# Optimization experiments

Measured on AMD Instinct MI355X. Metric: run time of the kernel, lower is better.

Reference implementation:

```python
import jax, jax.numpy as jnp
import numpy as np

B, N, IN_F, OUT_F = 32, 1024, 256, 256
ALPHA = 0.2  # LeakyReLU negative slope
NEG_INF = -9e15  # matches torch's -9000000000000000.0 masking constant


def setup_inputs() -> dict:
    key = jax.random.key(0)
    k1, k2, k3, k4 = jax.random.split(key, 4)
    h = jax.random.normal(k1, (B, N, IN_F), dtype=jnp.float32)
    adj = jax.random.randint(k2, (B, N, N), 0, 2, dtype=jnp.int32)
    W = jax.random.normal(k3, (OUT_F, IN_F), dtype=jnp.float32) * 0.05
    a = jax.random.normal(k4, (1, 2 * OUT_F), dtype=jnp.float32) * 0.05
    return {"h": h, "adj": adj, "W": W, "a": a}


def reference(h, adj, W, a):
    # Wh: (B, N, out)
    Wh = jnp.einsum("bni,oi->bno", h, W)
    # Decompose a([Wh_i || Wh_j]) = Wh_i . a1 + Wh_j . a2 (identical math,
    # avoids the O(B*N^2*2*out) concat intermediate of the torch code).
    a1 = a[0, :OUT_F]   # (out,)
    a2 = a[0, OUT_F:]   # (out,)
    si = Wh @ a1        # (B, N) score contribution of source node i
    sj = Wh @ a2        # (B, N) score contribution of neighbor node j
    e = jax.nn.leaky_relu(si[:, :, None] + sj[:, None, :], negative_slope=ALPHA)
    attention = jnp.where(adj > 0, e, NEG_INF)
    attention = jax.nn.softmax(attention, axis=-1)
    # dropout omitted (eval mode)
    h_prime = jnp.einsum("bij,bjo->bio", attention, Wh)
    return jax.nn.elu(h_prime)
```

## Files before the change

### kernel.cpp

```cpp
#include <hip/hip_runtime.h>
#include <hip/hip_bf16.h>


#define ALPHA 0.2f
#define LOG2E 1.44269504f

typedef __bf16 bf16x8 __attribute__((ext_vector_type(8)));
typedef __bf16 bf16x4 __attribute__((ext_vector_type(4)));
typedef float  f32x4  __attribute__((ext_vector_type(4)));
typedef unsigned long long u64;

__global__ __launch_bounds__(256) void k1_gemm1(const float* __restrict__ h,
                                                const float* __restrict__ W,
                                                const float* __restrict__ a_g,
                                                __bf16* __restrict__ whT,
                                                float* __restrict__ si,
                                                float* __restrict__ sj) {
    __shared__ __bf16 hA[64 * 72];
    __shared__ __bf16 hB[256 * 72];
    __shared__ float  red[512];
    const int t    = threadIdx.x;
    const int r0   = blockIdx.x * 64;
    const int b    = r0 >> 10;
    const int n0   = r0 & 1023;
    const int w    = t >> 6;
    const int l    = t & 63;
    const int ln   = l & 15;
    const int quad = l >> 4;

    f32x4 acc[4][4] = {};
    float4 ha_r[4], wb_r[16];

    #pragma unroll
    for (int it = 0; it < 4; ++it)
        ha_r[it] = *(const float4*)&h[(size_t)(r0 + it * 16 + (t >> 4)) * 256 + (t & 15) * 4];
    #pragma unroll
    for (int it = 0; it < 16; ++it)
        wb_r[it] = *(const float4*)&W[(size_t)(it * 16 + (t >> 4)) * 256 + (t & 15) * 4];

    for (int kc = 0; kc < 4; ++kc) {
        #pragma unroll
        for (int it = 0; it < 4; ++it) {
            const float4 v = ha_r[it];
            bf16x4 pv = {(__bf16)v.x, (__bf16)v.y, (__bf16)v.z, (__bf16)v.w};
            *(bf16x4*)&hA[(it * 16 + (t >> 4)) * 72 + (t & 15) * 4] = pv;
        }
        #pragma unroll
        for (int it = 0; it < 16; ++it) {
            const float4 v = wb_r[it];
            bf16x4 pv = {(__bf16)v.x, (__bf16)v.y, (__bf16)v.z, (__bf16)v.w};
            *(bf16x4*)&hB[(it * 16 + (t >> 4)) * 72 + (t & 15) * 4] = pv;
        }
        __syncthreads();
        if (kc < 3) {
            const int k0 = (kc + 1) * 64;
            #pragma unroll
            for (int it = 0; it < 4; ++it)
                ha_r[it] = *(const float4*)&h[(size_t)(r0 + it * 16 + (t >> 4)) * 256 + k0 + (t & 15) * 4];
            #pragma unroll
            for (int it = 0; it < 16; ++it)
                wb_r[it] = *(const float4*)&W[(size_t)(it * 16 + (t >> 4)) * 256 + k0 + (t & 15) * 4];
        }
        #pragma unroll
        for (int kk = 0; kk < 2; ++kk) {
            bf16x8 af[4], bfr[4];
            #pragma unroll
            for (int ri = 0; ri < 4; ++ri)
                af[ri] = *(const bf16x8*)&hA[(ri * 16 + ln) * 72 + kk * 32 + quad * 8];
            #pragma unroll
            for (int oi = 0; oi < 4; ++oi)
                bfr[oi] = *(const bf16x8*)&hB[(w * 64 + oi * 16 + ln) * 72 + kk * 32 + quad * 8];
            #pragma unroll
            for (int ri = 0; ri < 4; ++ri)
                #pragma unroll
                for (int oi = 0; oi < 4; ++oi)
                    acc[ri][oi] = __builtin_amdgcn_mfma_f32_16x16x32_bf16(
                        af[ri], bfr[oi], acc[ri][oi], 0, 0, 0);
        }
        __syncthreads();
    }

    #pragma unroll
    for (int ri = 0; ri < 4; ++ri) {
        const int n = ri * 16 + quad * 4;
        #pragma unroll
        for (int oi = 0; oi < 4; ++oi) {
            const int o = w * 64 + oi * 16 + ln;
            bf16x4 pv = {(__bf16)acc[ri][oi][0], (__bf16)acc[ri][oi][1],
                         (__bf16)acc[ri][oi][2], (__bf16)acc[ri][oi][3]};
            *(bf16x4*)&hB[o * 72 + n] = pv;
        }
    }
    __syncthreads();

    #pragma unroll
    for (int it = 0; it < 8; ++it) {
        const int o   = w * 64 + it * 8 + (l >> 3);
        const int seg = l & 7;
        const bf16x8 v = *(const bf16x8*)&hB[o * 72 + seg * 8];
        *(bf16x8*)&whT[((size_t)b * 256 + o) * 1024 + n0 + seg * 8] = v;
    }

    {
        float s1 = 0.f, s2 = 0.f;
        #pragma unroll 8
        for (int oi = 0; oi < 64; ++oi) {
            const int o = w * 64 + oi;
            const float v = (float)hB[o * 72 + l];
            s1 += v * a_g[o];
            s2 += v * a_g[256 + o];
        }
        red[w * 64 + l]       = s1;
        red[256 + w * 64 + l] = s2;
    }
    __syncthreads();
    if (t < 64) {
        si[b * 1024 + n0 + t] =
            (red[t] + red[64 + t] + red[128 + t] + red[192 + t]) * LOG2E;
    } else if (t < 128) {
        const int n = t - 64;
        sj[b * 1024 + n0 + n] =
            (red[256 + n] + red[320 + n] + red[384 + n] + red[448 + n]) * LOG2E;
    }
}

#define K3_BODY(JC, A0C, A1C, SJC, A0N, A1N, SJN)                              \
  {                                                                            \
    const int j0 = (JC) * 64;                                                  \
       \
    _Pragma("unroll")                                                          \
    for (int it = 0; it < 4; ++it)                                             \
      *(bf16x8*)&lds_w[(it * 64 + (t >> 3)) * 72 + (t & 7) * 8] = vreg[it];    \
              \
    if ((JC) < 15) {                                                           \
      _Pragma("unroll")                                                        \
      for (int it = 0; it < 4; ++it)                                           \
        vreg[it] = *(const bf16x8*)&whTb[                                      \
            (size_t)(it * 64 + (t >> 3)) * 1024 + j0 + 64 + (t & 7) * 8];      \
      A0N = *(const int4*)&adjb[(size_t)rowg * 1024 + j0 + 64 + j4 * 4];       \
      A1N = *(const int4*)&adjb[(size_t)(rowg + 32) * 1024 + j0 + 64 + j4 * 4];\
      SJN = *(const float4*)&sj_g[bs + j0 + 64 + j4 * 4];                      \
    }                                                                          \
         \
    {                                                                          \
      float e0 = si0 + SJC.x; e0 = fmaxf(e0, ALPHA * e0);                      \
      float e1 = si0 + SJC.y; e1 = fmaxf(e1, ALPHA * e1);                      \
      float e2 = si0 + SJC.z; e2 = fmaxf(e2, ALPHA * e2);                      \
      float e3 = si0 + SJC.w; e3 = fmaxf(e3, ALPHA * e3);                      \
      const float w0 = A0C.x > 0 ? exp2f(e0) : 0.f;                            \
      const float w1 = A0C.y > 0 ? exp2f(e1) : 0.f;                            \
      const float w2 = A0C.z > 0 ? exp2f(e2) : 0.f;                            \
      const float w3 = A0C.w > 0 ? exp2f(e3) : 0.f;                            \
      bf16x4 pv = {(__bf16)w0, (__bf16)w1, (__bf16)w2, (__bf16)w3};            \
      dsum0 += (float)pv[0] + (float)pv[1] + (float)pv[2] + (float)pv[3];      \
      *(bf16x4*)&lds_s[rowg * 72 + j4 * 4] = pv;                               \
    }                                                                          \
    {                                                                          \
      float e0 = si1 + SJC.x; e0 = fmaxf(e0, ALPHA * e0);                      \
      float e1 = si1 + SJC.y; e1 = fmaxf(e1, ALPHA * e1);                      \
      float e2 = si1 + SJC.z; e2 = fmaxf(e2, ALPHA * e2);                      \
      float e3 = si1 + SJC.w; e3 = fmaxf(e3, ALPHA * e3);                      \
      const float w0 = A1C.x > 0 ? exp2f(e0) : 0.f;                            \
      const float w1 = A1C.y > 0 ? exp2f(e1) : 0.f;                            \
      const float w2 = A1C.z > 0 ? exp2f(e2) : 0.f;                            \
      const float w3 = A1C.w > 0 ? exp2f(e3) : 0.f;                            \
      bf16x4 pv = {(__bf16)w0, (__bf16)w1, (__bf16)w2, (__bf16)w3};            \
      dsum1 += (float)pv[0] + (float)pv[1] + (float)pv[2] + (float)pv[3];      \
      *(bf16x4*)&lds_s[(rowg + 32) * 72 + j4 * 4] = pv;                        \
    }                                                                          \
    __syncthreads();                                                           \
                                \
    __builtin_amdgcn_s_setprio(1);                                             \
    _Pragma("unroll")                                                          \
    for (int kk = 0; kk < 2; ++kk) {                                           \
      bf16x8 af[4], bfr[2];                                                    \
      _Pragma("unroll")                                                        \
      for (int ri = 0; ri < 4; ++ri)                                           \
        af[ri] = *(const bf16x8*)&lds_s[(ri * 16 + ln) * 72 + kk * 32 + quad * 8]; \
      _Pragma("unroll")                                                        \
      for (int oi = 0; oi < 2; ++oi)                                           \
        bfr[oi] = *(const bf16x8*)&lds_w[(w * 32 + oi * 16 + ln) * 72 + kk * 32 + quad * 8]; \
      _Pragma("unroll")                                                        \
      for (int ri = 0; ri < 4; ++ri)                                           \
        _Pragma("unroll")                                                      \
        for (int oi = 0; oi < 2; ++oi)                                         \
          acc[ri][oi] = __builtin_amdgcn_mfma_f32_16x16x32_bf16(               \
              af[ri], bfr[oi], acc[ri][oi], 0, 0, 0);                          \
    }                                                                          \
    __builtin_amdgcn_s_setprio(0);                                             \
    __syncthreads();                                                           \
  }

__global__ __launch_bounds__(512, 4) void k3_attn(const int* __restrict__ adj,
                                                  const __bf16* __restrict__ whT,
                                                  const float* __restrict__ si_g,
                                                  const float* __restrict__ sj_g,
                                                  float* __restrict__ out) {
    __shared__ __bf16 lds_w[256 * 72];
    __shared__ __bf16 lds_s[64 * 72];
    __shared__ float  lds_denom[64];
    const int t = threadIdx.x;
    const int orig = blockIdx.x;
    const int wgid = (orig & 7) * 64 + (orig >> 3);
    const int b    = wgid >> 4;
    const int i0   = (wgid & 15) << 6;
    const int w    = t >> 6;
    const int l    = t & 63;
    const int ln   = l & 15;
    const int quad = l >> 4;
    const int rowg = t >> 4;
    const int j4   = t & 15;
    const int bs   = b * 1024;

    const float si0 = si_g[bs + i0 + rowg];
    const float si1 = si_g[bs + i0 + rowg + 32];

    float dsum0 = 0.f, dsum1 = 0.f;
    f32x4 acc[4][2] = {};
    const __bf16* whTb = whT + (size_t)b * 256 * 1024;
    const int*    adjb = adj + ((size_t)(bs + i0)) * 1024;

    bf16x8 vreg[4];
    int4   a0_c, a1_c, a0_n, a1_n;
    float4 sj_c, sj_n;

    #pragma unroll
    for (int it = 0; it < 4; ++it)
        vreg[it] = *(const bf16x8*)&whTb[(size_t)(it * 64 + (t >> 3)) * 1024 + (t & 7) * 8];
    a0_c = *(const int4*)&adjb[(size_t)rowg * 1024 + j4 * 4];
    a1_c = *(const int4*)&adjb[(size_t)(rowg + 32) * 1024 + j4 * 4];
    sj_c = *(const float4*)&sj_g[bs + j4 * 4];

    for (int jj = 0; jj < 8; ++jj) {
        K3_BODY(2 * jj,     a0_c, a1_c, sj_c, a0_n, a1_n, sj_n);
        K3_BODY(2 * jj + 1, a0_n, a1_n, sj_n, a0_c, a1_c, sj_c);
    }

    {
        float v = dsum0;
        v += __shfl_xor(v, 1);
        v += __shfl_xor(v, 2);
        v += __shfl_xor(v, 4);
        v += __shfl_xor(v, 8);
        if (j4 == 0) lds_denom[rowg] = v;
        float u = dsum1;
        u += __shfl_xor(u, 1);
        u += __shfl_xor(u, 2);
        u += __shfl_xor(u, 4);
        u += __shfl_xor(u, 8);
        if (j4 == 0) lds_denom[rowg + 32] = u;
    }
    __syncthreads();
    #pragma unroll
    for (int ri = 0; ri < 4; ++ri) {
        #pragma unroll
        for (int q = 0; q < 4; ++q) {
            const int il = ri * 16 + quad * 4 + q;
            const float dinv = 1.0f / fmaxf(lds_denom[il], 1e-30f);
            #pragma unroll
            for (int oi = 0; oi < 2; ++oi) {
                const int o = w * 32 + oi * 16 + ln;
                const float v = acc[ri][oi][q] * dinv;
                const float r = v > 0.f ? v : __expf(v) - 1.f;
                out[((size_t)(bs + i0 + il)) * 256 + o] = r;
            }
        }
    }
}

extern "C" void kernel_launch(void* const* d_in, const int* in_sizes, int n_in,
                              void* d_out, int out_size, void* d_ws, size_t ws_size,
                              hipStream_t stream) {
    const float* h   = (const float*)d_in[0];
    const int*   adj = (const int*)d_in[1];
    const float* W   = (const float*)d_in[2];
    const float* a   = (const float*)d_in[3];
    float* out = (float*)d_out;

    __bf16* whT = (__bf16*)d_ws;
    float*  si  = (float*)((char*)d_ws + (size_t)16777216);
    float*  sj  = (float*)((char*)d_ws + (size_t)16777216 + 131072);

    k1_gemm1<<<512, 256, 0, stream>>>(h, W, a, whT, si, sj);
    k3_attn<<<512, 512, 0, stream>>>(adj, whT, si, sj, out);
}
```

Before: 250.4 us.

## Split attention kernel into score phase into full-row LDS then barrier-free MFMA phase

The attention kernel is restructured into two phases. Phase one computes the masked exp weights for all 1024 columns of the block's 64 rows and stores them in a large LDS buffer. Phase two runs the MFMA GEMM, with each wave loading its Wh^T fragments straight from global memory into registers and double-buffering them, instead of staging Wh in LDS. This removes the per-tile LDS copy of Wh and the two barriers per tile. The cost is about 132KB of LDS per block, which sharply cuts occupancy, and phase one no longer overlaps with MFMA work.

```diff
diff --git a/kernel.cpp b/kernel.cpp
--- a/kernel.cpp
+++ b/kernel.cpp
@@ -124,24 +124,15 @@
     }
 }
 
-#define K3_BODY(JC, A0C, A1C, SJC, A0N, A1N, SJN)                              \
+
+#define P1_BODY(JC, A0C, A1C, SJC, A0N, A1N, SJN)                              \
   {                                                                            \
     const int j0 = (JC) * 64;                                                  \
-       \
-    _Pragma("unroll")                                                          \
-    for (int it = 0; it < 4; ++it)                                             \
-      *(bf16x8*)&lds_w[(it * 64 + (t >> 3)) * 72 + (t & 7) * 8] = vreg[it];    \
-              \
     if ((JC) < 15) {                                                           \
-      _Pragma("unroll")                                                        \
-      for (int it = 0; it < 4; ++it)                                           \
-        vreg[it] = *(const bf16x8*)&whTb[                                      \
-            (size_t)(it * 64 + (t >> 3)) * 1024 + j0 + 64 + (t & 7) * 8];      \
       A0N = *(const int4*)&adjb[(size_t)rowg * 1024 + j0 + 64 + j4 * 4];       \
       A1N = *(const int4*)&adjb[(size_t)(rowg + 32) * 1024 + j0 + 64 + j4 * 4];\
       SJN = *(const float4*)&sj_g[bs + j0 + 64 + j4 * 4];                      \
     }                                                                          \
-         \
     {                                                                          \
       float e0 = si0 + SJC.x; e0 = fmaxf(e0, ALPHA * e0);                      \
       float e1 = si0 + SJC.y; e1 = fmaxf(e1, ALPHA * e1);                      \
@@ -153,7 +144,7 @@
       const float w3 = A0C.w > 0 ? exp2f(e3) : 0.f;                            \
       bf16x4 pv = {(__bf16)w0, (__bf16)w1, (__bf16)w2, (__bf16)w3};            \
       dsum0 += (float)pv[0] + (float)pv[1] + (float)pv[2] + (float)pv[3];      \
-      *(bf16x4*)&lds_s[rowg * 72 + j4 * 4] = pv;                               \
+      *(bf16x4*)&lds_s[rowg * 1032 + j0 + j4 * 4] = pv;                        \
     }                                                                          \
     {                                                                          \
       float e0 = si1 + SJC.x; e0 = fmaxf(e0, ALPHA * e0);                      \
@@ -166,38 +157,38 @@
       const float w3 = A1C.w > 0 ? exp2f(e3) : 0.f;                            \
       bf16x4 pv = {(__bf16)w0, (__bf16)w1, (__bf16)w2, (__bf16)w3};            \
       dsum1 += (float)pv[0] + (float)pv[1] + (float)pv[2] + (float)pv[3];      \
-      *(bf16x4*)&lds_s[(rowg + 32) * 72 + j4 * 4] = pv;                        \
-    }                                                                          \
-    __syncthreads();                                                           \
-                                \
+      *(bf16x4*)&lds_s[(rowg + 32) * 1032 + j0 + j4 * 4] = pv;                 \
+    }                                                                          \
+  }
+
+#define P2_BODY(JS, B0C, B1C, B0N, B1N)                                        \
+  {                                                                            \
+    const int j0 = (JS) * 32;                                                  \
+    if ((JS) < 31) {                                                           \
+      B0N = *(const bf16x8*)&whTb[(size_t)(oc + ln) * 1024 + j0 + 32 + quad * 8];      \
+      B1N = *(const bf16x8*)&whTb[(size_t)(oc + 16 + ln) * 1024 + j0 + 32 + quad * 8]; \
+    }                                                                          \
+    bf16x8 af[4];                                                              \
+    _Pragma("unroll")                                                          \
+    for (int ri = 0; ri < 4; ++ri)                                             \
+      af[ri] = *(const bf16x8*)&lds_s[(ri * 16 + ln) * 1032 + j0 + quad * 8];  \
     __builtin_amdgcn_s_setprio(1);                                             \
     _Pragma("unroll")                                                          \
-    for (int kk = 0; kk < 2; ++kk) {                                           \
-      bf16x8 af[4], bfr[2];                                                    \
-      _Pragma("unroll")                                                        \
-      for (int ri = 0; ri < 4; ++ri)                                           \
-        af[ri] = *(const bf16x8*)&lds_s[(ri * 16 + ln) * 72 + kk * 32 + quad * 8]; \
-      _Pragma("unroll")                                                        \
-      for (int oi = 0; oi < 2; ++oi)                                           \
-        bfr[oi] = *(const bf16x8*)&lds_w[(w * 32 + oi * 16 + ln) * 72 + kk * 32 + quad * 8]; \
-      _Pragma("unroll")                                                        \
-      for (int ri = 0; ri < 4; ++ri)                                           \
-        _Pragma("unroll")                                                      \
-        for (int oi = 0; oi < 2; ++oi)                                         \
-          acc[ri][oi] = __builtin_amdgcn_mfma_f32_16x16x32_bf16(               \
-              af[ri], bfr[oi], acc[ri][oi], 0, 0, 0);                          \
+    for (int ri = 0; ri < 4; ++ri) {                                           \
+      acc[ri][0] = __builtin_amdgcn_mfma_f32_16x16x32_bf16(af[ri], B0C,        \
+                                                           acc[ri][0], 0, 0, 0); \
+      acc[ri][1] = __builtin_amdgcn_mfma_f32_16x16x32_bf16(af[ri], B1C,        \
+                                                           acc[ri][1], 0, 0, 0); \
     }                                                                          \
     __builtin_amdgcn_s_setprio(0);                                             \
-    __syncthreads();                                                           \
   }
 
-__global__ __launch_bounds__(512, 4) void k3_attn(const int* __restrict__ adj,
-                                                  const __bf16* __restrict__ whT,
-                                                  const float* __restrict__ si_g,
-                                                  const float* __restrict__ sj_g,
-                                                  float* __restrict__ out) {
-    __shared__ __bf16 lds_w[256 * 72];
-    __shared__ __bf16 lds_s[64 * 72];
+__global__ __launch_bounds__(512) void k3_attn(const int* __restrict__ adj,
+                                               const __bf16* __restrict__ whT,
+                                               const float* __restrict__ si_g,
+                                               const float* __restrict__ sj_g,
+                                               float* __restrict__ out) {
+    __shared__ __bf16 lds_s[64 * 1032];
     __shared__ float  lds_denom[64];
     const int t = threadIdx.x;
     const int orig = blockIdx.x;
@@ -211,29 +202,24 @@
     const int rowg = t >> 4;
     const int j4   = t & 15;
     const int bs   = b * 1024;
+    const int oc   = w * 32;
 
     const float si0 = si_g[bs + i0 + rowg];
     const float si1 = si_g[bs + i0 + rowg + 32];
 
     float dsum0 = 0.f, dsum1 = 0.f;
-    f32x4 acc[4][2] = {};
     const __bf16* whTb = whT + (size_t)b * 256 * 1024;
     const int*    adjb = adj + ((size_t)(bs + i0)) * 1024;
 
-    bf16x8 vreg[4];
     int4   a0_c, a1_c, a0_n, a1_n;
     float4 sj_c, sj_n;
-
-    #pragma unroll
-    for (int it = 0; it < 4; ++it)
-        vreg[it] = *(const bf16x8*)&whTb[(size_t)(it * 64 + (t >> 3)) * 1024 + (t & 7) * 8];
     a0_c = *(const int4*)&adjb[(size_t)rowg * 1024 + j4 * 4];
     a1_c = *(const int4*)&adjb[(size_t)(rowg + 32) * 1024 + j4 * 4];
     sj_c = *(const float4*)&sj_g[bs + j4 * 4];
 
     for (int jj = 0; jj < 8; ++jj) {
-        K3_BODY(2 * jj,     a0_c, a1_c, sj_c, a0_n, a1_n, sj_n);
-        K3_BODY(2 * jj + 1, a0_n, a1_n, sj_n, a0_c, a1_c, sj_c);
+        P1_BODY(2 * jj,     a0_c, a1_c, sj_c, a0_n, a1_n, sj_n);
+        P1_BODY(2 * jj + 1, a0_n, a1_n, sj_n, a0_c, a1_c, sj_c);
     }
 
     {
@@ -250,7 +236,19 @@
         u += __shfl_xor(u, 8);
         if (j4 == 0) lds_denom[rowg + 32] = u;
     }
+
     __syncthreads();
+
+    f32x4 acc[4][2] = {};
+    bf16x8 b0_c, b1_c, b0_n, b1_n;
+    b0_c = *(const bf16x8*)&whTb[(size_t)(oc + ln) * 1024 + quad * 8];
+    b1_c = *(const bf16x8*)&whTb[(size_t)(oc + 16 + ln) * 1024 + quad * 8];
+
+    for (int ss = 0; ss < 16; ++ss) {
+        P2_BODY(2 * ss,     b0_c, b1_c, b0_n, b1_n);
+        P2_BODY(2 * ss + 1, b0_n, b1_n, b0_c, b1_c);
+    }
+
     #pragma unroll
     for (int ri = 0; ri < 4; ++ri) {
         #pragma unroll
@@ -259,7 +257,7 @@
             const float dinv = 1.0f / fmaxf(lds_denom[il], 1e-30f);
             #pragma unroll
             for (int oi = 0; oi < 2; ++oi) {
-                const int o = w * 32 + oi * 16 + ln;
+                const int o = oc + oi * 16 + ln;
                 const float v = acc[ri][oi][q] * dinv;
                 const float r = v > 0.f ? v : __expf(v) - 1.f;
                 out[((size_t)(bs + i0 + il)) * 256 + o] = r;
```

Result: slower. 276.6 us (+10.4%).

## Software-pipeline attention score computation one tile ahead of MFMA stage

Applied to the files above, without the earlier changes.

The exp/leaky-relu score values for the next 64-column tile are now computed in registers while the current tile's MFMA work proceeds. Only a store of the precomputed values to LDS sits before the barrier. Adjacency and sj loads are prefetched two tiles ahead to feed this deeper pipeline. The aim is to overlap VALU/transcendental work with matrix-core work and shorten the critical path before each sync, at the cost of extra live registers, which may lower occupancy.

```diff
diff --git a/kernel.cpp b/kernel.cpp
--- a/kernel.cpp
+++ b/kernel.cpp
@@ -124,52 +124,55 @@
     }
 }
 
-#define K3_BODY(JC, A0C, A1C, SJC, A0N, A1N, SJN)                              \
+
+#define SVAL_PAIR(PN0, PN1, A0, A1, SJ)                                        \
   {                                                                            \
-    const int j0 = (JC) * 64;                                                  \
-       \
+    float e0 = si0 + SJ.x; e0 = fmaxf(e0, ALPHA * e0);                         \
+    float e1 = si0 + SJ.y; e1 = fmaxf(e1, ALPHA * e1);                         \
+    float e2 = si0 + SJ.z; e2 = fmaxf(e2, ALPHA * e2);                         \
+    float e3 = si0 + SJ.w; e3 = fmaxf(e3, ALPHA * e3);                         \
+    const float w0 = A0.x > 0 ? exp2f(e0) : 0.f;                               \
+    const float w1 = A0.y > 0 ? exp2f(e1) : 0.f;                               \
+    const float w2 = A0.z > 0 ? exp2f(e2) : 0.f;                               \
+    const float w3 = A0.w > 0 ? exp2f(e3) : 0.f;                               \
+    PN0 = (bf16x4){(__bf16)w0, (__bf16)w1, (__bf16)w2, (__bf16)w3};            \
+    dsum0 += (float)PN0[0] + (float)PN0[1] + (float)PN0[2] + (float)PN0[3];    \
+    float f0 = si1 + SJ.x; f0 = fmaxf(f0, ALPHA * f0);                         \
+    float f1 = si1 + SJ.y; f1 = fmaxf(f1, ALPHA * f1);                         \
+    float f2 = si1 + SJ.z; f2 = fmaxf(f2, ALPHA * f2);                         \
+    float f3 = si1 + SJ.w; f3 = fmaxf(f3, ALPHA * f3);                         \
+    const float u0 = A1.x > 0 ? exp2f(f0) : 0.f;                               \
+    const float u1 = A1.y > 0 ? exp2f(f1) : 0.f;                               \
+    const float u2 = A1.z > 0 ? exp2f(f2) : 0.f;                               \
+    const float u3 = A1.w > 0 ? exp2f(f3) : 0.f;                               \
+    PN1 = (bf16x4){(__bf16)u0, (__bf16)u1, (__bf16)u2, (__bf16)u3};            \
+    dsum1 += (float)PN1[0] + (float)PN1[1] + (float)PN1[2] + (float)PN1[3];    \
+  }
+
+#define K3_ITER(C, PC0, PC1, PN0, PN1, AC0, AC1, SJC, AN0, AN1, SJN)           \
+  {                                                                            \
+    const int j0 = (C) * 64;                                                   \
+          \
     _Pragma("unroll")                                                          \
     for (int it = 0; it < 4; ++it)                                             \
       *(bf16x8*)&lds_w[(it * 64 + (t >> 3)) * 72 + (t & 7) * 8] = vreg[it];    \
-              \
-    if ((JC) < 15) {                                                           \
+    *(bf16x4*)&lds_s[rowg * 72 + j4 * 4] = PC0;                                \
+    *(bf16x4*)&lds_s[(rowg + 32) * 72 + j4 * 4] = PC1;                         \
+    __syncthreads();                                                           \
+         \
+    if ((C) < 15) {                                                            \
       _Pragma("unroll")                                                        \
       for (int it = 0; it < 4; ++it)                                           \
         vreg[it] = *(const bf16x8*)&whTb[                                      \
             (size_t)(it * 64 + (t >> 3)) * 1024 + j0 + 64 + (t & 7) * 8];      \
-      A0N = *(const int4*)&adjb[(size_t)rowg * 1024 + j0 + 64 + j4 * 4];       \
-      A1N = *(const int4*)&adjb[(size_t)(rowg + 32) * 1024 + j0 + 64 + j4 * 4];\
-      SJN = *(const float4*)&sj_g[bs + j0 + 64 + j4 * 4];                      \
+      SVAL_PAIR(PN0, PN1, AC0, AC1, SJC);                                      \
+      if ((C) < 14) {                                                          \
+        const int jr = j0 + 128 + j4 * 4;                                      \
+        AN0 = *(const int4*)&adjb[(size_t)rowg * 1024 + jr];                   \
+        AN1 = *(const int4*)&adjb[(size_t)(rowg + 32) * 1024 + jr];            \
+        SJN = *(const float4*)&sj_g[bs + jr];                                  \
+      }                                                                        \
     }                                                                          \
-         \
-    {                                                                          \
-      float e0 = si0 + SJC.x; e0 = fmaxf(e0, ALPHA * e0);                      \
-      float e1 = si0 + SJC.y; e1 = fmaxf(e1, ALPHA * e1);                      \
-      float e2 = si0 + SJC.z; e2 = fmaxf(e2, ALPHA * e2);                      \
-      float e3 = si0 + SJC.w; e3 = fmaxf(e3, ALPHA * e3);                      \
-      const float w0 = A0C.x > 0 ? exp2f(e0) : 0.f;                            \
-      const float w1 = A0C.y > 0 ? exp2f(e1) : 0.f;                            \
-      const float w2 = A0C.z > 0 ? exp2f(e2) : 0.f;                            \
-      const float w3 = A0C.w > 0 ? exp2f(e3) : 0.f;                            \
-      bf16x4 pv = {(__bf16)w0, (__bf16)w1, (__bf16)w2, (__bf16)w3};            \
-      dsum0 += (float)pv[0] + (float)pv[1] + (float)pv[2] + (float)pv[3];      \
-      *(bf16x4*)&lds_s[rowg * 72 + j4 * 4] = pv;                               \
-    }                                                                          \
-    {                                                                          \
-      float e0 = si1 + SJC.x; e0 = fmaxf(e0, ALPHA * e0);                      \
-      float e1 = si1 + SJC.y; e1 = fmaxf(e1, ALPHA * e1);                      \
-      float e2 = si1 + SJC.z; e2 = fmaxf(e2, ALPHA * e2);                      \
-      float e3 = si1 + SJC.w; e3 = fmaxf(e3, ALPHA * e3);                      \
-      const float w0 = A1C.x > 0 ? exp2f(e0) : 0.f;                            \
-      const float w1 = A1C.y > 0 ? exp2f(e1) : 0.f;                            \
-      const float w2 = A1C.z > 0 ? exp2f(e2) : 0.f;                            \
-      const float w3 = A1C.w > 0 ? exp2f(e3) : 0.f;                            \
-      bf16x4 pv = {(__bf16)w0, (__bf16)w1, (__bf16)w2, (__bf16)w3};            \
-      dsum1 += (float)pv[0] + (float)pv[1] + (float)pv[2] + (float)pv[3];      \
-      *(bf16x4*)&lds_s[(rowg + 32) * 72 + j4 * 4] = pv;                        \
-    }                                                                          \
-    __syncthreads();                                                           \
-                                \
     __builtin_amdgcn_s_setprio(1);                                             \
     _Pragma("unroll")                                                          \
     for (int kk = 0; kk < 2; ++kk) {                                           \
@@ -221,6 +224,7 @@
     const int*    adjb = adj + ((size_t)(bs + i0)) * 1024;
 
     bf16x8 vreg[4];
+    bf16x4 pvA0, pvA1, pvB0, pvB1;
     int4   a0_c, a1_c, a0_n, a1_n;
     float4 sj_c, sj_n;
 
@@ -230,10 +234,16 @@
     a0_c = *(const int4*)&adjb[(size_t)rowg * 1024 + j4 * 4];
     a1_c = *(const int4*)&adjb[(size_t)(rowg + 32) * 1024 + j4 * 4];
     sj_c = *(const float4*)&sj_g[bs + j4 * 4];
+    SVAL_PAIR(pvA0, pvA1, a0_c, a1_c, sj_c);
+    a0_c = *(const int4*)&adjb[(size_t)rowg * 1024 + 64 + j4 * 4];
+    a1_c = *(const int4*)&adjb[(size_t)(rowg + 32) * 1024 + 64 + j4 * 4];
+    sj_c = *(const float4*)&sj_g[bs + 64 + j4 * 4];
 
     for (int jj = 0; jj < 8; ++jj) {
-        K3_BODY(2 * jj,     a0_c, a1_c, sj_c, a0_n, a1_n, sj_n);
-        K3_BODY(2 * jj + 1, a0_n, a1_n, sj_n, a0_c, a1_c, sj_c);
+        K3_ITER(2 * jj,     pvA0, pvA1, pvB0, pvB1,
+                            a0_c, a1_c, sj_c, a0_n, a1_n, sj_n);
+        K3_ITER(2 * jj + 1, pvB0, pvB1, pvA0, pvA1,
+                            a0_n, a1_n, sj_n, a0_c, a1_c, sj_c);
     }
 
     {
```

Result: no change. 253.1 us (+1.1%).
